# Kernel optimization log

Measured on AMD Instinct MI355X. Metric: run time of the kernel, lower is better.

The kernel has to match this reference:

```python
import jax, jax.numpy as jnp
import numpy as np

B, L, D, H = 2, 2048, 1024, 16
HD = D // H
SCALE = HD ** -0.5


def setup_inputs() -> dict:
    key = jax.random.key(0)
    ks = jax.random.split(key, 11)
    s = D ** -0.5  # torch Linear default init scale (uniform bound)
    return {
        "q": jax.random.normal(ks[0], (B, L, D), jnp.float32),
        "k": jax.random.normal(ks[1], (B, L, D), jnp.float32),
        "v": jax.random.normal(ks[2], (B, L, D), jnp.float32),
        "Wq": jax.random.uniform(ks[3], (D, D), jnp.float32, -s, s),
        "bq": jax.random.uniform(ks[4], (D,), jnp.float32, -s, s),
        "Wk": jax.random.uniform(ks[5], (D, D), jnp.float32, -s, s),
        "bk": jax.random.uniform(ks[6], (D,), jnp.float32, -s, s),
        "Wv": jax.random.uniform(ks[7], (D, D), jnp.float32, -s, s),
        "bv": jax.random.uniform(ks[8], (D,), jnp.float32, -s, s),
        "Wo": jax.random.uniform(ks[9], (D, D), jnp.float32, -s, s),
        "bo": jax.random.uniform(ks[10], (D,), jnp.float32, -s, s),
    }


def reference(q, k, v, Wq, bq, Wk, bk, Wv, bv, Wo, bo):
    b, q_len, _ = q.shape
    # projections; weights stored as (D, D) acting on the right: x @ W + b
    qh = (q @ Wq + bq).reshape(b, q_len, H, HD).transpose(0, 2, 1, 3)  # (B,H,Q,hd)
    kh = (k @ Wk + bk).reshape(b, -1, H, HD).transpose(0, 2, 1, 3)    # (B,H,K,hd)
    vh = (v @ Wv + bv).reshape(b, -1, H, HD).transpose(0, 2, 1, 3)    # (B,H,K,hd)
    att = jnp.einsum("bhqd,bhkd->bhqk", qh * SCALE, kh)               # (B,H,Q,K)
    att = jax.nn.softmax(att, axis=-1)
    out = jnp.einsum("bhqk,bhkd->bhqd", att, vh)                      # (B,H,Q,hd)
    out = out.transpose(0, 2, 1, 3).reshape(b, q_len, D)
    return out @ Wo + bo
```

## Files before the change

kernel.cpp:

```cpp
#include <hip/hip_runtime.h>

namespace {
constexpr int kB  = 2;
constexpr int kL  = 2048;
constexpr int kD  = 1024;
constexpr int kH  = 16;
constexpr int kHD = 64;
constexpr int kM  = kB * kL;
}

typedef _Float16 f16x8 __attribute__((ext_vector_type(8)));
typedef float    f32x16 __attribute__((ext_vector_type(16)));
typedef unsigned int u32;

union Frag16 { uint4 u4; unsigned u[4]; f16x8 v; };

__device__ __forceinline__ unsigned short f2h(float f) {
    return __builtin_bit_cast(unsigned short, (_Float16)f);
}

__device__ __forceinline__ void gload16(const void* g, void* l) {
    __builtin_amdgcn_global_load_lds(
        (const __attribute__((address_space(1))) u32*)g,
        (__attribute__((address_space(3))) u32*)(unsigned long long)(__builtin_bit_cast(unsigned long long, l)),
        16, 0, 0);
}

__global__ __launch_bounds__(256) void cast_f16_kernel(
    const float* __restrict__ q, const float* __restrict__ k,
    const float* __restrict__ v, unsigned short* __restrict__ dst)
{
    const float* src = blockIdx.y == 0 ? q : (blockIdx.y == 1 ? k : v);
    unsigned short* d = dst + (size_t)blockIdx.y * ((size_t)kM * kD);
    const size_t i = ((size_t)blockIdx.x * 256 + threadIdx.x) * 8;
    const float4 f0 = *(const float4*)(src + i);
    const float4 f1 = *(const float4*)(src + i + 4);
    _Float16 h[8];
    h[0] = (_Float16)f0.x; h[1] = (_Float16)f0.y;
    h[2] = (_Float16)f0.z; h[3] = (_Float16)f0.w;
    h[4] = (_Float16)f1.x; h[5] = (_Float16)f1.y;
    h[6] = (_Float16)f1.z; h[7] = (_Float16)f1.w;
    *(uint4*)(d + i) = *(uint4*)h;
}

__global__ __launch_bounds__(256) void tcast_kernel(
    const float* __restrict__ W0, const float* __restrict__ W1,
    const float* __restrict__ W2, const float* __restrict__ W3,
    unsigned short* __restrict__ WtBase)
{
    __shared__ _Float16 T[64][68];
    const float* W = blockIdx.z == 0 ? W0 : blockIdx.z == 1 ? W1
                   : blockIdx.z == 2 ? W2 : W3;
    unsigned short* Wt = WtBase + (size_t)blockIdx.z * ((size_t)kD * kD);
    const int k0 = blockIdx.y * 64, n0 = blockIdx.x * 64;
    const int tx = threadIdx.x & 15, ty = threadIdx.x >> 4;
#pragma unroll
    for (int i = 0; i < 4; ++i) {
        const int kk = i * 16 + ty;
        const float4 w = *(const float4*)&W[(size_t)(k0 + kk) * kD + n0 + tx * 4];
        T[tx * 4 + 0][kk] = (_Float16)w.x;
        T[tx * 4 + 1][kk] = (_Float16)w.y;
        T[tx * 4 + 2][kk] = (_Float16)w.z;
        T[tx * 4 + 3][kk] = (_Float16)w.w;
    }
    __syncthreads();
#pragma unroll
    for (int i = 0; i < 4; ++i) {
        const int nn = i * 16 + ty;
        *(ushort4*)&Wt[(size_t)(n0 + nn) * kD + k0 + tx * 4] = *(ushort4*)&T[nn][tx * 4];
    }
}

template <int MODE>
__global__ __launch_bounds__(256) void gemm16_kernel(
    const unsigned short* __restrict__ A, const unsigned short* __restrict__ Wt,
    const float* __restrict__ bias, void* __restrict__ Cv)
{
    __shared__ unsigned short Als[2][128 * 64];
    __shared__ unsigned short Bls[2][128 * 64];

    const int tid = threadIdx.x;
    const int lane = tid & 63;
    const int wid = tid >> 6;
    const int l31 = lane & 31;
    const int hi = lane >> 5;
    const int by = blockIdx.x & 31;
    const int bx = blockIdx.x >> 5;
    const int row0 = by * 128;
    const int col0 = bx * 128;
    const int wr = wid >> 1, wc = wid & 1;

    const int rl = lane >> 3;
    const int sl = lane & 7;
    const int ssrc = (sl ^ rl) * 8;

    const unsigned short* Abase = A + (size_t)(row0 + wid * 32 + rl) * kD + ssrc;
    const unsigned short* Bbase = Wt + (size_t)(col0 + wid * 32 + rl) * kD + ssrc;

    f32x16 acc00{}, acc01{}, acc10{}, acc11{};

    auto stage = [&](int kt, int buf) {
#pragma unroll
        for (int i = 0; i < 4; ++i) {
            gload16(Abase + (size_t)(i * 8) * kD + kt * 64,
                    &Als[buf][(wid * 32 + i * 8) * 64]);
        }
#pragma unroll
        for (int i = 0; i < 4; ++i) {
            gload16(Bbase + (size_t)(i * 8) * kD + kt * 64,
                    &Bls[buf][(wid * 32 + i * 8) * 64]);
        }
    };

    const int ra0 = wr * 64 + l31;
    const int cb0 = wc * 64 + l31;

    stage(0, 0);
    int cur = 0;
    for (int kt = 0; kt < kD / 64; ++kt) {
        __syncthreads();
        if (kt + 1 < kD / 64) stage(kt + 1, cur ^ 1);
#pragma unroll
        for (int ks = 0; ks < 4; ++ks) {
            const int slot = (ks << 1) | hi;
            Frag16 a0, a1, b0, b1;
            a0.u4 = *(const uint4*)&Als[cur][ra0 * 64 + ((slot ^ (ra0 & 7)) << 3)];
            a1.u4 = *(const uint4*)&Als[cur][(ra0 + 32) * 64 + ((slot ^ ((ra0 + 32) & 7)) << 3)];
            b0.u4 = *(const uint4*)&Bls[cur][cb0 * 64 + ((slot ^ (cb0 & 7)) << 3)];
            b1.u4 = *(const uint4*)&Bls[cur][(cb0 + 32) * 64 + ((slot ^ ((cb0 + 32) & 7)) << 3)];
            acc00 = __builtin_amdgcn_mfma_f32_32x32x16_f16(a0.v, b0.v, acc00, 0, 0, 0);
            acc01 = __builtin_amdgcn_mfma_f32_32x32x16_f16(a0.v, b1.v, acc01, 0, 0, 0);
            acc10 = __builtin_amdgcn_mfma_f32_32x32x16_f16(a1.v, b0.v, acc10, 0, 0, 0);
            acc11 = __builtin_amdgcn_mfma_f32_32x32x16_f16(a1.v, b1.v, acc11, 0, 0, 0);
        }
        cur ^= 1;
    }

    const float bias0 = bias[col0 + wc * 64 + l31];
    const float bias1 = bias[col0 + wc * 64 + 32 + l31];

    const f32x16* accs[2][2] = {{&acc00, &acc01}, {&acc10, &acc11}};
#pragma unroll
    for (int rt = 0; rt < 2; ++rt) {
#pragma unroll
        for (int ct = 0; ct < 2; ++ct) {
            const f32x16& acv = *accs[rt][ct];
            const float bb = ct ? bias1 : bias0;
            const int c = col0 + wc * 64 + ct * 32 + l31;
            if (MODE == 2) {
                unsigned short* C = (unsigned short*)Cv;
#pragma unroll
                for (int qd = 0; qd < 4; ++qd) {
                    const int r = row0 + wr * 64 + rt * 32 + 8 * qd + 4 * hi;
                    const int b_ = r >> 11, l_ = r & (kL - 1);
                    ushort4 w;
                    w.x = f2h(acv[4 * qd + 0] + bb);
                    w.y = f2h(acv[4 * qd + 1] + bb);
                    w.z = f2h(acv[4 * qd + 2] + bb);
                    w.w = f2h(acv[4 * qd + 3] + bb);
                    *(ushort4*)&C[((size_t)(b_ * kH + (c >> 6)) * kHD + (c & 63)) * kL + l_] = w;
                }
            } else {
#pragma unroll
                for (int reg = 0; reg < 16; ++reg) {
                    const int r = row0 + wr * 64 + rt * 32 + (reg & 3) + 8 * (reg >> 2) + 4 * hi;
                    const float val = acv[reg] + bb;
                    if (MODE == 0) {
                        ((float*)Cv)[(size_t)r * kD + c] = val;
                    } else {
                        const int b_ = r >> 11, l_ = r & (kL - 1);
                        ((unsigned short*)Cv)[((size_t)(b_ * kH + (c >> 6)) * kL + l_) * kHD + (c & 63)] = f2h(val);
                    }
                }
            }
        }
    }
}

__global__ __launch_bounds__(256) void attn_mfma_kernel(
    const unsigned short* __restrict__ Qh, const unsigned short* __restrict__ Kh,
    const unsigned short* __restrict__ Vt, unsigned short* __restrict__ O16)
{
    __shared__ unsigned short Kls[2][64 * 64];
    __shared__ unsigned short Vls[2][64 * 64];

    const int lane = threadIdx.x & 63;
    const int wid  = threadIdx.x >> 6;
    const int l31  = lane & 31;
    const int hi   = lane >> 5;
    const int qt = blockIdx.x, bh = blockIdx.y;
    const int q = qt * 128 + wid * 32 + l31;

    const size_t qkBase = (size_t)bh * kL * kHD;
    const unsigned short* Qp = Qh + qkBase + (size_t)q * kHD + hi * 8;
    Frag16 qf[4];
#pragma unroll
    for (int d = 0; d < 4; ++d) qf[d].u4 = *(const uint4*)(Qp + d * 16);

    const int srow = wid * 16 + (lane >> 3);
    const int sslot = lane & 7;
    const int soff = ((sslot ^ (srow & 7)) << 3);
    const unsigned short* Kg = Kh + qkBase + (size_t)srow * kHD + soff;
    const unsigned short* Vg = Vt + (size_t)bh * kHD * kL + (size_t)srow * kL + soff;

    auto stage = [&](int kt, int buf) {
        gload16(Kg + (size_t)(kt * 64) * kHD,            &Kls[buf][(wid * 16) * 64]);
        gload16(Kg + (size_t)(kt * 64 + 8) * kHD,        &Kls[buf][(wid * 16 + 8) * 64]);
        gload16(Vg + kt * 64,                            &Vls[buf][(wid * 16) * 64]);
        gload16(Vg + kt * 64 + (size_t)8 * kL,           &Vls[buf][(wid * 16 + 8) * 64]);
    };

    f32x16 o0{}, o1{};
    float m = -1e30f, lsum = 0.f;
    const float cexp = 0.125f * 1.44269504089f;

    stage(0, 0);
    int cur = 0;
    for (int kt = 0; kt < kL / 64; ++kt) {
        __syncthreads();
        if (kt + 1 < kL / 64) stage(kt + 1, cur ^ 1);

        const int rA = l31, rB = l31 + 32;
        f32x16 c0{}, c1{};
        Frag16 kf0[4], kf1[4];
#pragma unroll
        for (int d = 0; d < 4; ++d) {
            const int s = (d << 1) | hi;
            kf0[d].u4 = *(const uint4*)&Kls[cur][rA * 64 + ((s ^ (rA & 7)) << 3)];
            kf1[d].u4 = *(const uint4*)&Kls[cur][rB * 64 + ((s ^ (rB & 7)) << 3)];
        }
        Frag16 vf0[4], vf1[4];
#pragma unroll
        for (int ks = 0; ks < 4; ++ks) {
            const int s = (ks << 1) | hi;
            vf0[ks].u4 = *(const uint4*)&Vls[cur][rA * 64 + ((s ^ (rA & 7)) << 3)];
            vf1[ks].u4 = *(const uint4*)&Vls[cur][rB * 64 + ((s ^ (rB & 7)) << 3)];
        }
        __builtin_amdgcn_s_setprio(1);
#pragma unroll
        for (int d = 0; d < 4; ++d) {
            c0 = __builtin_amdgcn_mfma_f32_32x32x16_f16(kf0[d].v, qf[d].v, c0, 0, 0, 0);
            c1 = __builtin_amdgcn_mfma_f32_32x32x16_f16(kf1[d].v, qf[d].v, c1, 0, 0, 0);
        }
        __builtin_amdgcn_s_setprio(0);

        float mx = fmaxf(c0[0], c1[0]);
#pragma unroll
        for (int r = 1; r < 16; ++r) mx = fmaxf(mx, fmaxf(c0[r], c1[r]));
        mx = fmaxf(mx, __shfl_xor(mx, 32));
        if (mx > m + 48.f) {
            const float corr = __builtin_amdgcn_exp2f((m - mx) * cexp);
            m = mx;
            lsum *= corr;
            o0 *= corr;
            o1 *= corr;
        }
        const float mc = m * cexp;
        float p0[16], p1[16];
        float rs = 0.f;
#pragma unroll
        for (int r = 0; r < 16; ++r) {
            p0[r] = __builtin_amdgcn_exp2f(fmaf(c0[r], cexp, -mc));
            p1[r] = __builtin_amdgcn_exp2f(fmaf(c1[r], cexp, -mc));
            rs += p0[r] + p1[r];
        }
        rs += __shfl_xor(rs, 32);
        lsum += rs;

        unsigned u0[8], u1[8];
#pragma unroll
        for (int i = 0; i < 8; ++i) {
            union { _Float16 h[2]; unsigned w; } t;
            t.h[0] = (_Float16)p0[2 * i]; t.h[1] = (_Float16)p0[2 * i + 1];
            u0[i] = t.w;
            t.h[0] = (_Float16)p1[2 * i]; t.h[1] = (_Float16)p1[2 * i + 1];
            u1[i] = t.w;
        }
        Frag16 pf[4];
        {
            unsigned t0 = hi ? u0[0] : u0[2];
            unsigned t1 = hi ? u0[1] : u0[3];
            unsigned t2 = hi ? u0[4] : u0[6];
            unsigned t3 = hi ? u0[5] : u0[7];
            const unsigned r0 = __shfl_xor(t0, 32);
            const unsigned r1 = __shfl_xor(t1, 32);
            const unsigned r2 = __shfl_xor(t2, 32);
            const unsigned r3 = __shfl_xor(t3, 32);
            pf[0].u[0] = hi ? r0 : u0[0];
            pf[0].u[1] = hi ? r1 : u0[1];
            pf[0].u[2] = hi ? u0[2] : r0;
            pf[0].u[3] = hi ? u0[3] : r1;
            pf[1].u[0] = hi ? r2 : u0[4];
            pf[1].u[1] = hi ? r3 : u0[5];
            pf[1].u[2] = hi ? u0[6] : r2;
            pf[1].u[3] = hi ? u0[7] : r3;
        }
        {
            unsigned t0 = hi ? u1[0] : u1[2];
            unsigned t1 = hi ? u1[1] : u1[3];
            unsigned t2 = hi ? u1[4] : u1[6];
            unsigned t3 = hi ? u1[5] : u1[7];
            const unsigned r0 = __shfl_xor(t0, 32);
            const unsigned r1 = __shfl_xor(t1, 32);
            const unsigned r2 = __shfl_xor(t2, 32);
            const unsigned r3 = __shfl_xor(t3, 32);
            pf[2].u[0] = hi ? r0 : u1[0];
            pf[2].u[1] = hi ? r1 : u1[1];
            pf[2].u[2] = hi ? u1[2] : r0;
            pf[2].u[3] = hi ? u1[3] : r1;
            pf[3].u[0] = hi ? r2 : u1[4];
            pf[3].u[1] = hi ? r3 : u1[5];
            pf[3].u[2] = hi ? u1[6] : r2;
            pf[3].u[3] = hi ? u1[7] : r3;
        }

        __builtin_amdgcn_s_setprio(1);
#pragma unroll
        for (int ks = 0; ks < 4; ++ks) {
            o0 = __builtin_amdgcn_mfma_f32_32x32x16_f16(vf0[ks].v, pf[ks].v, o0, 0, 0, 0);
            o1 = __builtin_amdgcn_mfma_f32_32x32x16_f16(vf1[ks].v, pf[ks].v, o1, 0, 0, 0);
        }
        __builtin_amdgcn_s_setprio(0);
        cur ^= 1;
    }

    const float inv = 1.f / lsum;
    const int b_ = bh >> 4, h_ = bh & 15;
    unsigned short* outp = O16 + ((size_t)(b_ * kL + q)) * kD + h_ * kHD;
#pragma unroll
    for (int g = 0; g < 4; ++g) {
        const int d = g * 8 + hi * 4;
        ushort4 w0, w1;
        w0.x = f2h(o0[4 * g + 0] * inv); w0.y = f2h(o0[4 * g + 1] * inv);
        w0.z = f2h(o0[4 * g + 2] * inv); w0.w = f2h(o0[4 * g + 3] * inv);
        w1.x = f2h(o1[4 * g + 0] * inv); w1.y = f2h(o1[4 * g + 1] * inv);
        w1.z = f2h(o1[4 * g + 2] * inv); w1.w = f2h(o1[4 * g + 3] * inv);
        *(ushort4*)(outp + d) = w0;
        *(ushort4*)(outp + 32 + d) = w1;
    }
}

extern "C" void kernel_launch(void* const* d_in, const int* in_sizes, int n_in,
                              void* d_out, int out_size, void* d_ws, size_t ws_size,
                              hipStream_t stream)
{
    const float* q  = (const float*)d_in[0];
    const float* k  = (const float*)d_in[1];
    const float* v  = (const float*)d_in[2];
    const float* Wq = (const float*)d_in[3];
    const float* bq = (const float*)d_in[4];
    const float* Wk = (const float*)d_in[5];
    const float* bk = (const float*)d_in[6];
    const float* Wv = (const float*)d_in[7];
    const float* bv = (const float*)d_in[8];
    const float* Wo = (const float*)d_in[9];
    const float* bo = (const float*)d_in[10];
    float* out = (float*)d_out;

    const size_t MD = (size_t)kM * kD;
    const size_t DD = (size_t)kD * kD;
    unsigned short* A16 = (unsigned short*)d_ws;
    unsigned short* Wt16 = A16 + 3 * MD;
    unsigned short* Qh16 = Wt16 + 4 * DD;
    unsigned short* Kh16 = Qh16 + MD;
    unsigned short* Vt16 = Kh16 + MD;
    unsigned short* O16  = A16;

    const dim3 blk(256);

    hipLaunchKernelGGL(cast_f16_kernel, dim3(kM * kD / (256 * 8), 3), blk, 0, stream,
                       q, k, v, A16);
    hipLaunchKernelGGL(tcast_kernel, dim3(16, 16, 4), blk, 0, stream,
                       Wq, Wk, Wv, Wo, Wt16);

    hipLaunchKernelGGL((gemm16_kernel<1>), dim3(256), blk, 0, stream,
                       A16, Wt16, bq, (void*)Qh16);
    hipLaunchKernelGGL((gemm16_kernel<1>), dim3(256), blk, 0, stream,
                       A16 + MD, Wt16 + DD, bk, (void*)Kh16);
    hipLaunchKernelGGL((gemm16_kernel<2>), dim3(256), blk, 0, stream,
                       A16 + 2 * MD, Wt16 + 2 * DD, bv, (void*)Vt16);

    hipLaunchKernelGGL(attn_mfma_kernel, dim3(kL / 128, kB * kH), blk, 0, stream,
                       Qh16, Kh16, Vt16, O16);

    hipLaunchKernelGGL((gemm16_kernel<0>), dim3(256), blk, 0, stream,
                       O16, Wt16 + 3 * DD, bo, (void*)out);
}
```

Measured before the change: 147.5 us.

## Split attention over two key halves and merge partial outputs

The attention kernel now splits the key range into two halves, launching a 1D grid of 1024 blocks instead of 512. The block index is remapped so blocks sharing a head are grouped. Each block writes a normalized fp16 partial output plus its (max, sum) statistics, and a new merge kernel rescales and combines the two halves into the head-interleaved layout. The intent is to raise the number of resident waves per CU and hide latency, at the cost of an extra launch, partial-output traffic, and extra fp16 rounding. Float-to-half packing also switches to the cvt_pkrtz intrinsic.

```diff
diff --git a/kernel.cpp b/kernel.cpp
--- a/kernel.cpp
+++ b/kernel.cpp
@@ -10,6 +10,7 @@
 }
 
 typedef _Float16 f16x8 __attribute__((ext_vector_type(8)));
+typedef _Float16 f16x2 __attribute__((ext_vector_type(2)));
 typedef float    f32x16 __attribute__((ext_vector_type(16)));
 typedef unsigned int u32;
 
@@ -17,6 +18,9 @@
 
 __device__ __forceinline__ unsigned short f2h(float f) {
     return __builtin_bit_cast(unsigned short, (_Float16)f);
+}
+__device__ __forceinline__ unsigned pk2(float a, float b) {
+    return __builtin_bit_cast(unsigned, __builtin_amdgcn_cvt_pkrtz(a, b));
 }
 
 __device__ __forceinline__ void gload16(const void* g, void* l) {
@@ -179,7 +183,8 @@
 
 __global__ __launch_bounds__(256) void attn_mfma_kernel(
     const unsigned short* __restrict__ Qh, const unsigned short* __restrict__ Kh,
-    const unsigned short* __restrict__ Vt, unsigned short* __restrict__ O16)
+    const unsigned short* __restrict__ Vt, unsigned short* __restrict__ Opart,
+    float2* __restrict__ Stat)
 {
     __shared__ unsigned short Kls[2][64 * 64];
     __shared__ unsigned short Vls[2][64 * 64];
@@ -188,7 +193,12 @@
     const int wid  = threadIdx.x >> 6;
     const int l31  = lane & 31;
     const int hi   = lane >> 5;
-    const int qt = blockIdx.x, bh = blockIdx.y;
+
+    const int id = blockIdx.x;
+    const int j  = id >> 3;
+    const int bh = (id & 7) * 4 + (j >> 5);
+    const int qt = j & 15;
+    const int ks = (j >> 4) & 1;
     const int q = qt * 128 + wid * 32 + l31;
 
     const size_t qkBase = (size_t)bh * kL * kHD;
@@ -198,27 +208,27 @@
     for (int d = 0; d < 4; ++d) qf[d].u4 = *(const uint4*)(Qp + d * 16);
 
     const int srow = wid * 16 + (lane >> 3);
-    const int sslot = lane & 7;
-    const int soff = ((sslot ^ (srow & 7)) << 3);
+    const int soff = (((lane & 7) ^ (srow & 7)) << 3);
     const unsigned short* Kg = Kh + qkBase + (size_t)srow * kHD + soff;
     const unsigned short* Vg = Vt + (size_t)bh * kHD * kL + (size_t)srow * kL + soff;
 
     auto stage = [&](int kt, int buf) {
-        gload16(Kg + (size_t)(kt * 64) * kHD,            &Kls[buf][(wid * 16) * 64]);
-        gload16(Kg + (size_t)(kt * 64 + 8) * kHD,        &Kls[buf][(wid * 16 + 8) * 64]);
-        gload16(Vg + kt * 64,                            &Vls[buf][(wid * 16) * 64]);
-        gload16(Vg + kt * 64 + (size_t)8 * kL,           &Vls[buf][(wid * 16 + 8) * 64]);
+        gload16(Kg + (size_t)(kt * 64) * kHD,     &Kls[buf][(wid * 16) * 64]);
+        gload16(Kg + (size_t)(kt * 64 + 8) * kHD, &Kls[buf][(wid * 16 + 8) * 64]);
+        gload16(Vg + kt * 64,                     &Vls[buf][(wid * 16) * 64]);
+        gload16(Vg + kt * 64 + (size_t)8 * kL,    &Vls[buf][(wid * 16 + 8) * 64]);
     };
 
     f32x16 o0{}, o1{};
     float m = -1e30f, lsum = 0.f;
     const float cexp = 0.125f * 1.44269504089f;
 
-    stage(0, 0);
+    const int kt0 = ks * 16;
+    stage(kt0, 0);
     int cur = 0;
-    for (int kt = 0; kt < kL / 64; ++kt) {
+    for (int lt = 0; lt < 16; ++lt) {
         __syncthreads();
-        if (kt + 1 < kL / 64) stage(kt + 1, cur ^ 1);
+        if (lt + 1 < 16) stage(kt0 + lt + 1, cur ^ 1);
 
         const int rA = l31, rB = l31 + 32;
         f32x16 c0{}, c1{};
@@ -231,10 +241,10 @@
         }
         Frag16 vf0[4], vf1[4];
 #pragma unroll
-        for (int ks = 0; ks < 4; ++ks) {
-            const int s = (ks << 1) | hi;
-            vf0[ks].u4 = *(const uint4*)&Vls[cur][rA * 64 + ((s ^ (rA & 7)) << 3)];
-            vf1[ks].u4 = *(const uint4*)&Vls[cur][rB * 64 + ((s ^ (rB & 7)) << 3)];
+        for (int ksl = 0; ksl < 4; ++ksl) {
+            const int s = (ksl << 1) | hi;
+            vf0[ksl].u4 = *(const uint4*)&Vls[cur][rA * 64 + ((s ^ (rA & 7)) << 3)];
+            vf1[ksl].u4 = *(const uint4*)&Vls[cur][rB * 64 + ((s ^ (rB & 7)) << 3)];
         }
         __builtin_amdgcn_s_setprio(1);
 #pragma unroll
@@ -270,11 +280,8 @@
         unsigned u0[8], u1[8];
 #pragma unroll
         for (int i = 0; i < 8; ++i) {
-            union { _Float16 h[2]; unsigned w; } t;
-            t.h[0] = (_Float16)p0[2 * i]; t.h[1] = (_Float16)p0[2 * i + 1];
-            u0[i] = t.w;
-            t.h[0] = (_Float16)p1[2 * i]; t.h[1] = (_Float16)p1[2 * i + 1];
-            u1[i] = t.w;
+            u0[i] = pk2(p0[2 * i], p0[2 * i + 1]);
+            u1[i] = pk2(p1[2 * i], p1[2 * i + 1]);
         }
         Frag16 pf[4];
         {
@@ -316,28 +323,64 @@
 
         __builtin_amdgcn_s_setprio(1);
 #pragma unroll
-        for (int ks = 0; ks < 4; ++ks) {
-            o0 = __builtin_amdgcn_mfma_f32_32x32x16_f16(vf0[ks].v, pf[ks].v, o0, 0, 0, 0);
-            o1 = __builtin_amdgcn_mfma_f32_32x32x16_f16(vf1[ks].v, pf[ks].v, o1, 0, 0, 0);
+        for (int ksl = 0; ksl < 4; ++ksl) {
+            o0 = __builtin_amdgcn_mfma_f32_32x32x16_f16(vf0[ksl].v, pf[ksl].v, o0, 0, 0, 0);
+            o1 = __builtin_amdgcn_mfma_f32_32x32x16_f16(vf1[ksl].v, pf[ksl].v, o1, 0, 0, 0);
         }
         __builtin_amdgcn_s_setprio(0);
         cur ^= 1;
     }
 
+    const size_t prow = (size_t)ks * (32 * kL) + (size_t)bh * kL + q;
     const float inv = 1.f / lsum;
-    const int b_ = bh >> 4, h_ = bh & 15;
-    unsigned short* outp = O16 + ((size_t)(b_ * kL + q)) * kD + h_ * kHD;
+    unsigned short* pp = Opart + prow * kHD;
 #pragma unroll
     for (int g = 0; g < 4; ++g) {
         const int d = g * 8 + hi * 4;
-        ushort4 w0, w1;
-        w0.x = f2h(o0[4 * g + 0] * inv); w0.y = f2h(o0[4 * g + 1] * inv);
-        w0.z = f2h(o0[4 * g + 2] * inv); w0.w = f2h(o0[4 * g + 3] * inv);
-        w1.x = f2h(o1[4 * g + 0] * inv); w1.y = f2h(o1[4 * g + 1] * inv);
-        w1.z = f2h(o1[4 * g + 2] * inv); w1.w = f2h(o1[4 * g + 3] * inv);
-        *(ushort4*)(outp + d) = w0;
-        *(ushort4*)(outp + 32 + d) = w1;
-    }
+        uint2 w0, w1;
+        w0.x = pk2(o0[4 * g + 0] * inv, o0[4 * g + 1] * inv);
+        w0.y = pk2(o0[4 * g + 2] * inv, o0[4 * g + 3] * inv);
+        w1.x = pk2(o1[4 * g + 0] * inv, o1[4 * g + 1] * inv);
+        w1.y = pk2(o1[4 * g + 2] * inv, o1[4 * g + 3] * inv);
+        *(uint2*)(pp + d) = w0;
+        *(uint2*)(pp + 32 + d) = w1;
+    }
+    if (hi == 0) Stat[prow] = make_float2(m, lsum);
+}
+
+__global__ __launch_bounds__(256) void merge_kernel(
+    const unsigned short* __restrict__ Opart, const float2* __restrict__ Stat,
+    unsigned short* __restrict__ O16)
+{
+    const int g = blockIdx.x * 256 + threadIdx.x;
+    const int row = g >> 3;
+    const int d0 = (g & 7) * 8;
+    const int bh = row >> 11, q = row & (kL - 1);
+    const float2 sa = Stat[row];
+    const float2 sb = Stat[32 * kL + row];
+    const float cexp = 0.125f * 1.44269504089f;
+    const float M = fmaxf(sa.x, sb.x);
+    float wa = __builtin_amdgcn_exp2f((sa.x - M) * cexp) * sa.y;
+    float wb = __builtin_amdgcn_exp2f((sb.x - M) * cexp) * sb.y;
+    const float inv = 1.f / (wa + wb);
+    wa *= inv; wb *= inv;
+
+    const unsigned short* pa = Opart + (size_t)row * kHD + d0;
+    const unsigned short* pb = pa + (size_t)32 * kL * kHD;
+    uint4 ua = *(const uint4*)pa;
+    uint4 ub = *(const uint4*)pb;
+    _Float16 ha[8], hb[8];
+    *(uint4*)ha = ua;
+    *(uint4*)hb = ub;
+    unsigned out[4];
+#pragma unroll
+    for (int i = 0; i < 4; ++i) {
+        const float v0 = wa * (float)ha[2 * i]     + wb * (float)hb[2 * i];
+        const float v1 = wa * (float)ha[2 * i + 1] + wb * (float)hb[2 * i + 1];
+        out[i] = pk2(v0, v1);
+    }
+    const int b_ = bh >> 4, h_ = bh & 15;
+    *(uint4*)&O16[((size_t)(b_ * kL + q)) * kD + h_ * kHD + d0] = *(uint4*)out;
 }
 
 extern "C" void kernel_launch(void* const* d_in, const int* in_sizes, int n_in,
@@ -364,7 +407,9 @@
     unsigned short* Qh16 = Wt16 + 4 * DD;
     unsigned short* Kh16 = Qh16 + MD;
     unsigned short* Vt16 = Kh16 + MD;
-    unsigned short* O16  = A16;
+    unsigned short* O16   = A16;
+    unsigned short* Opart = A16 + MD;
+    float2*         Stat  = (float2*)Wt16;
 
     const dim3 blk(256);
 
@@ -380,8 +425,10 @@
     hipLaunchKernelGGL((gemm16_kernel<2>), dim3(256), blk, 0, stream,
                        A16 + 2 * MD, Wt16 + 2 * DD, bv, (void*)Vt16);
 
-    hipLaunchKernelGGL(attn_mfma_kernel, dim3(kL / 128, kB * kH), blk, 0, stream,
-                       Qh16, Kh16, Vt16, O16);
+    hipLaunchKernelGGL(attn_mfma_kernel, dim3(1024), blk, 0, stream,
+                       Qh16, Kh16, Vt16, Opart, Stat);
+    hipLaunchKernelGGL(merge_kernel, dim3(2048), blk, 0, stream,
+                       Opart, Stat, O16);
 
     hipLaunchKernelGGL((gemm16_kernel<0>), dim3(256), blk, 0, stream,
                        O16, Wt16 + 3 * DD, bo, (void*)out);
```

Result: no change. 148.4 us (+0.6%).
